# Optimization experiments

Measured on AMD Instinct MI355X. Metric: run time of the kernel, lower is better.

The kernel has to match this reference:

```python
import jax, jax.numpy as jnp
import numpy as np

B, S, D, H, NATT = 8, 512, 768, 256, 11  # batch, seq, d_model, gru hidden, n attention branches


def setup_inputs() -> dict:
    key = jax.random.key(0)
    ks = jax.random.split(key, 20)
    w = lambda k, shp, s=0.02: (jax.random.normal(k, shp, jnp.float32) * s)
    emb = w(ks[0], (7, D), 1.0).at[0].set(0.0)  # padding_idx=0 row is zero
    return {
        "essay_amlabel": jax.random.randint(ks[1], (B, S), 0, 7),
        "sequence_output": jax.random.normal(ks[2], (B, S, D), jnp.float32),
        "emb_table": emb,
        "Wq": w(ks[3], (NATT, D, D)), "bq": jnp.zeros((NATT, D), jnp.float32),
        "Wk": w(ks[4], (NATT, D, D)), "bk": jnp.zeros((NATT, D), jnp.float32),
        "Wv": w(ks[5], (NATT, D, D)), "bv": jnp.zeros((NATT, D), jnp.float32),
        "gru_Wih": w(ks[6], (2, 3 * H, D), 1.0 / np.sqrt(H)),
        "gru_Whh": w(ks[7], (2, 3 * H, H), 1.0 / np.sqrt(H)),
        "gru_bih": jnp.zeros((2, 3 * H), jnp.float32),
        "gru_bhh": jnp.zeros((2, 3 * H), jnp.float32),
        "W1": w(ks[8], (2 * H, 1)), "b1": jnp.zeros((1,), jnp.float32),
    }


def _gru_final_hidden(x, Wih, Whh, bih, bhh, reverse):
    # x: [N, S, D] -> final hidden [N, H] (PyTorch GRU equations)
    xp = jnp.einsum('nsd,hd->snh', x, Wih) + bih  # [S, N, 3H]

    def step(h, xt):
        gh = h @ Whh.T + bhh
        i_r, i_z, i_n = jnp.split(xt, 3, axis=-1)
        h_r, h_z, h_n = jnp.split(gh, 3, axis=-1)
        r = jax.nn.sigmoid(i_r + h_r)
        z = jax.nn.sigmoid(i_z + h_z)
        n = jnp.tanh(i_n + r * h_n)
        h_new = (1.0 - z) * n + z * h
        return h_new, None

    h0 = jnp.zeros((x.shape[0], Whh.shape[1]), x.dtype)
    h_final, _ = jax.lax.scan(step, h0, xp, reverse=reverse)
    return h_final


def reference(essay_amlabel, sequence_output, emb_table, Wq, bq, Wk, bk, Wv, bv,
              gru_Wih, gru_Whh, gru_bih, gru_bhh, W1, b1):
    am = emb_table[essay_amlabel]  # [B, S, D] queries
    # 11 independent attentions, num_heads=1, dropout=0 (eval) -> stack on axis k
    Q = jax.nn.relu(jnp.einsum('bsd,kde->kbse', am, Wq) + bq[:, None, None, :])
    K = jax.nn.relu(jnp.einsum('bsd,kde->kbse', sequence_output, Wk) + bk[:, None, None, :])
    V = jax.nn.relu(jnp.einsum('bsd,kde->kbse', sequence_output, Wv) + bv[:, None, None, :])
    scores = jnp.einsum('kbqd,kbmd->kbqm', Q, K) / jnp.sqrt(jnp.float32(D))
    attn = jax.nn.softmax(scores, axis=-1)
    qmask = jnp.sign(jnp.abs(jnp.sum(am, axis=-1)))  # [B, S]
    attn = attn * qmask[None, :, :, None]  # post-softmax query mask (as in source)
    out = jnp.einsum('kbqm,kbmd->kbqd', attn, V) + am[None]  # residual with queries
    eloutput = out + sequence_output[None]  # [11, B, S, D]
    gru_in = eloutput.reshape(NATT * B, S, D)
    h_f = _gru_final_hidden(gru_in, gru_Wih[0], gru_Whh[0], gru_bih[0], gru_bhh[0], False)
    h_b = _gru_final_hidden(gru_in, gru_Wih[1], gru_Whh[1], gru_bih[1], gru_bhh[1], True)
    final = jnp.concatenate([h_f, h_b], axis=-1)  # [11B, 2H]
    reshaped = final.reshape(NATT, B, 2 * H).transpose(1, 0, 2)  # [B, 11, 2H]
    logits = jax.nn.sigmoid(reshaped @ W1 + b1).squeeze(-1)  # [B, 11]
    return logits
```

## Files before the change

### kernel.cpp

```cpp
#include <hip/hip_runtime.h>
#include <hip/hip_bf16.h>
#include <hip/hip_fp16.h>
#include <math.h>

typedef __hip_bfloat16 bf16;
typedef __attribute__((ext_vector_type(8))) short short8;
typedef __attribute__((ext_vector_type(4))) float f32x4;

#define NATT 11
#define Bb 8
#define Ss 512
#define Dd 768
#define Hh 256
#define WSLICE 589824L

__device__ __forceinline__ void stf(float* p, float v) { *p = v; }
__device__ __forceinline__ void stf(bf16* p, float v) { *p = __float2bfloat16(v); }

__device__ __forceinline__ float blo(unsigned u) { return __uint_as_float(u << 16); }
__device__ __forceinline__ float bhi(unsigned u) { return __uint_as_float(u & 0xffff0000u); }
__device__ __forceinline__ float b2f(unsigned short u) { return __uint_as_float(((unsigned)u) << 16); }

__device__ __forceinline__ float ldg_any(const void* base, long idx, int flag) {
  if (flag) return ((const float*)base)[idx];
  return __bfloat162float(((const bf16*)base)[idx]);
}

__device__ __forceinline__ unsigned packh2(float a, float b) {
  __half2 hh = __floats2half2_rn(a, b);
  return __builtin_bit_cast(unsigned, hh);
}
__device__ __forceinline__ unsigned short f2h(float v) {
  __half h = __float2half(v);
  return __builtin_bit_cast(unsigned short, h);
}

typedef _Float16 f16x2 __attribute__((ext_vector_type(2)));

__device__ __forceinline__ float dot2u(unsigned a, unsigned b, float c) {
#if __has_builtin(__builtin_amdgcn_fdot2)
  return __builtin_amdgcn_fdot2(__builtin_bit_cast(f16x2, a),
                                __builtin_bit_cast(f16x2, b), c, false);
#else
  __half2 ah = __builtin_bit_cast(__half2, a);
  __half2 bh = __builtin_bit_cast(__half2, b);
  float2 af = __half22float2(ah), bf = __half22float2(bh);
  return c + af.x * bf.x + af.y * bf.y;
#endif
}

__device__ __forceinline__ float quad_sum(float v) {
#if __has_builtin(__builtin_amdgcn_update_dpp)
  int y = __builtin_amdgcn_update_dpp(0, __builtin_bit_cast(int, v), 0xB1, 0xF, 0xF, true);
  v += __builtin_bit_cast(float, y);
  y = __builtin_amdgcn_update_dpp(0, __builtin_bit_cast(int, v), 0x4E, 0xF, 0xF, true);
  v += __builtin_bit_cast(float, y);
  return v;
#else
  v += __shfl_xor(v, 1);
  v += __shfl_xor(v, 2);
  return v;
#endif
}

__device__ __forceinline__ void lds_barrier() {
  asm volatile("s_waitcnt lgkmcnt(0)\n\ts_barrier" ::: "memory");
}

__device__ __forceinline__ void load_lds16(const void* g, void* l) {
  __builtin_amdgcn_global_load_lds(
      (const __attribute__((address_space(1))) unsigned int*)g,
      (__attribute__((address_space(3))) unsigned int*)l, 16, 0, 0);
}

__global__ __launch_bounds__(64) void probe_kernel(
    const unsigned short* __restrict__ sequ, const unsigned* __restrict__ labu,
    int* __restrict__ flags)
{
  int t = threadIdx.x;
  int wild = 0;
#pragma unroll
  for (int i = 0; i < 4; i++) {
    unsigned short v = sequ[t + i * 64];
    int e = (v >> 7) & 0xFF;
    if (e < 90 || e > 160) wild++;
  }
  int nzodd = 0;
#pragma unroll
  for (int i = 0; i < 2; i++) {
    unsigned w = labu[(t + i * 64) * 2 + 1];
    if (w != 0) nzodd++;
  }
  for (int o = 32; o > 0; o >>= 1) {
    wild  += __shfl_down(wild, o);
    nzodd += __shfl_down(nzodd, o);
  }
  if (t == 0) {
    flags[0] = (wild > 32) ? 1 : 0;
    flags[1] = (nzodd == 0) ? 1 : 0;
  }
}

__global__ __launch_bounds__(256) void conv_seq_kernel(
    const void* __restrict__ seq, bf16* __restrict__ seqb,
    const int* __restrict__ flags)
{
  int flag = flags[0];
  long row = blockIdx.x;
#pragma unroll
  for (int i = 0; i < 3; i++) {
    long e = row * Dd + threadIdx.x + i * 256;
    seqb[e] = __float2bfloat16(ldg_any(seq, e, flag));
  }
}

__global__ __launch_bounds__(256) void convert_kernel(
    const void* __restrict__ src, bf16* __restrict__ dst, long n,
    const int* __restrict__ flags)
{
  int flag = flags[0];
  long i = (long)blockIdx.x * 256 + threadIdx.x;
  if (i < n) dst[i] = __float2bfloat16(ldg_any(src, i, flag));
}

__global__ __launch_bounds__(256) void smalls_kernel(
    const void* __restrict__ emb, const void* __restrict__ Wq,
    const void* __restrict__ bq, float* __restrict__ Qsmall,
    const int* __restrict__ flags)
{
  int flag = flags[0];
  __shared__ float embsh[7 * 768];
  int z = blockIdx.y, chunk = blockIdx.x, tid = threadIdx.x;
  for (int i = tid; i < 7 * 768; i += 256) embsh[i] = ldg_any(emb, i, flag);
  __syncthreads();
  int n = chunk * 256 + tid;
  float acc[7] = {};
  long base = (long)z * WSLICE;
  for (int e = 0; e < Dd; e++) {
    float wv = ldg_any(Wq, base + (long)e * Dd + n, flag);
#pragma unroll
    for (int l = 0; l < 7; l++) acc[l] += embsh[l * 768 + e] * wv;
  }
  float bv = ldg_any(bq, z * Dd + n, flag);
#pragma unroll
  for (int l = 0; l < 7; l++)
    Qsmall[((long)z * 7 + l) * Dd + n] = fmaxf(acc[l] + bv, 0.f);
}

__global__ __launch_bounds__(256) void emb_copy_kernel(
    const void* __restrict__ emb, bf16* __restrict__ outsm,
    float* __restrict__ qmask7, const int* __restrict__ flags)
{
  int flag = flags[0];
  int l = blockIdx.x;
  int t = threadIdx.x;
  float s = 0.f;
#pragma unroll
  for (int i = 0; i < 3; i++) {
    int e = t + i * 256;
    float v = ldg_any(emb, (long)l * Dd + e, flag);
    outsm[(long)(640 + l) * Dd + e] = __float2bfloat16(v);
    s += v;
  }
  for (int o = 32; o > 0; o >>= 1) s += __shfl_down(s, o);
  __shared__ float red[4];
  if ((t & 63) == 0) red[t >> 6] = s;
  __syncthreads();
  if (t == 0) {
    float tot = red[0] + red[1] + red[2] + red[3];
    qmask7[l] = (tot != 0.f) ? 1.f : 0.f;
  }
}

__global__ __launch_bounds__(256) void transpose2_kernel(
    const void* __restrict__ Wk, const void* __restrict__ Wv,
    bf16* __restrict__ WT, const int* __restrict__ flags)
{
  int flag = flags[0];
  __shared__ float tile[32][33];
  int z = blockIdx.z;
  int m = z >> 1, wsel = z & 1;
  const void* src = wsel ? Wv : Wk;
  long off = (long)m * WSLICE;
  bf16* dst = WT + (long)z * WSLICE;
  int kk0 = blockIdx.y * 32, n0 = blockIdx.x * 32;
  int tx = threadIdx.x & 31, ty = threadIdx.x >> 5;
#pragma unroll
  for (int i = 0; i < 4; i++)
    tile[ty + i * 8][tx] = ldg_any(src, off + (long)(kk0 + ty + i * 8) * Dd + n0 + tx, flag);
  __syncthreads();
#pragma unroll
  for (int i = 0; i < 4; i++)
    dst[(long)(n0 + ty + i * 8) * Dd + kk0 + tx] = __float2bfloat16(tile[tx][ty + i * 8]);
}

__device__ __forceinline__ void gemm_mfma_core(
    const bf16* __restrict__ Ab, long ldA,
    const bf16* __restrict__ Bbp, long ldB,
    bf16* As, bf16* Bs, int bm, int bn, int K,
    const void* bias, long bOff,
    void* C, long ldC, int cMode,
    float scale, int relu, int fflag)
{
  int tid = threadIdx.x;
  int lane = tid & 63, w = tid >> 6;
  int mo = (w & 1) * 64, no = (w >> 1) * 64;
  int l15 = lane & 15, q4 = lane >> 4;
  int gr = lane >> 2;
  int gs = (lane & 3) * 8;
  const bf16* aS0 = Ab + (long)(bm + w * 16 + gr) * ldA + gs;
  const bf16* aS1 = aS0 + 64 * ldA;
  const bf16* bS0 = Bbp + (long)(bn + w * 16 + gr) * ldB + gs;
  const bf16* bS1 = bS0 + 64 * ldB;
  bf16* aD0 = As + w * 512;
  bf16* aD1 = As + 2048 + w * 512;
  bf16* bD0 = Bs + w * 512;
  bf16* bD1 = Bs + 2048 + w * 512;

  f32x4 acc[4][4];
#pragma unroll
  for (int i = 0; i < 4; i++)
#pragma unroll
    for (int j = 0; j < 4; j++)
#pragma unroll
      for (int r = 0; r < 4; r++) acc[i][j][r] = 0.f;

  for (int k0 = 0; k0 < K; k0 += 32) {
    load_lds16(aS0, aD0);
    load_lds16(aS1, aD1);
    load_lds16(bS0, bD0);
    load_lds16(bS1, bD1);
    aS0 += 32; aS1 += 32; bS0 += 32; bS1 += 32;
    __syncthreads();
    short8 af[4], bfv[4];
#pragma unroll
    for (int i = 0; i < 4; i++)
      af[i] = *(const short8*)(As + (mo + i * 16 + l15) * 32 + q4 * 8);
#pragma unroll
    for (int j = 0; j < 4; j++)
      bfv[j] = *(const short8*)(Bs + (no + j * 16 + l15) * 32 + q4 * 8);
#pragma unroll
    for (int i = 0; i < 4; i++)
#pragma unroll
      for (int j = 0; j < 4; j++)
        acc[i][j] = __builtin_amdgcn_mfma_f32_16x16x32_bf16(af[i], bfv[j], acc[i][j], 0, 0, 0);
    __syncthreads();
  }

  float bsv[4];
#pragma unroll
  for (int j = 0; j < 4; j++) {
    int colg = bn + no + j * 16 + l15;
    bsv[j] = bias ? ldg_any(bias, bOff + colg, fflag) : 0.f;
  }
#pragma unroll
  for (int i = 0; i < 4; i++) {
#pragma unroll
    for (int j = 0; j < 4; j++) {
      int colg = bn + no + j * 16 + l15;
      if (cMode == 4) {
        int rowg0 = bm + mo + i * 16 + q4 * 4;
        ushort4 pk;
        unsigned short tmp[4];
#pragma unroll
        for (int r = 0; r < 4; r++) {
          float v = acc[i][j][r] * scale + bsv[j];
          if (relu) v = fmaxf(v, 0.f);
          tmp[r] = f2h(v);
        }
        pk.x = tmp[0]; pk.y = tmp[1]; pk.z = tmp[2]; pk.w = tmp[3];
        *(ushort4*)((unsigned short*)C + (long)colg * ldC + rowg0) = pk;
      } else {
#pragma unroll
        for (int r = 0; r < 4; r++) {
          int rowg = bm + mo + i * 16 + q4 * 4 + r;
          float v = acc[i][j][r] * scale + bsv[j];
          if (relu) v = fmaxf(v, 0.f);
          long off2 = (long)rowg * ldC + colg;
          if (cMode == 2)      ((float*)C)[off2] = v;
          else if (cMode == 3) ((unsigned short*)C)[off2] = f2h(v);
          else                 ((bf16*)C)[off2] = __float2bfloat16(v);
        }
      }
    }
  }
}

__global__ __launch_bounds__(256, 2) void proj_kernel(
    const bf16* __restrict__ seqb, const bf16* __restrict__ WT,
    const void* __restrict__ bk, const void* __restrict__ bv,
    unsigned short* __restrict__ Kb, unsigned short* __restrict__ Vt,
    const int* __restrict__ flags)
{
  __shared__ __align__(16) bf16 As[4096];
  __shared__ __align__(16) bf16 Bs[4096];
  int z = blockIdx.z;
  int m = z >> 1, wsel = z & 1;
  const bf16* B = WT + (long)z * WSLICE;
  if (wsel == 0) {
    gemm_mfma_core(seqb, Dd, B, Dd, As, Bs, blockIdx.y * 128, blockIdx.x * 128, Dd,
                   bk, (long)m * Dd, Kb + (long)m * 4096 * Dd, Dd, 3, 1.f, 1, flags[0]);
  } else {
    gemm_mfma_core(seqb, Dd, B, Dd, As, Bs, blockIdx.y * 128, blockIdx.x * 128, Dd,
                   bv, (long)m * Dd, Vt + (long)m * Dd * 4096, 4096, 4, 1.f, 1, flags[0]);
  }
}

__global__ __launch_bounds__(256, 2) void seqw_kernel(
    const bf16* __restrict__ seqb, const bf16* __restrict__ WihB,
    const void* __restrict__ bih, bf16* __restrict__ seqW,
    const int* __restrict__ flags)
{
  __shared__ __align__(16) bf16 As[4096];
  __shared__ __align__(16) bf16 Bs[4096];
  int dir = blockIdx.z;
  gemm_mfma_core(seqb, Dd, WihB + (long)dir * WSLICE, Dd, As, Bs,
                 blockIdx.y * 128, blockIdx.x * 128, Dd,
                 bih, (long)dir * Dd, seqW + (long)dir * 4096 * Dd, Dd, 0,
                 1.f, 0, flags[0]);
}

__global__ __launch_bounds__(256, 2) void pvw_kernel(
    const bf16* __restrict__ outsm, const bf16* __restrict__ WihB,
    float* __restrict__ PVW, const int* __restrict__ flags)
{
  __shared__ __align__(16) bf16 As[4096];
  __shared__ __align__(16) bf16 Bs[4096];
  int dir = blockIdx.z;
  gemm_mfma_core(outsm, Dd, WihB + (long)dir * WSLICE, Dd, As, Bs,
                 blockIdx.y * 128, blockIdx.x * 128, Dd,
                 nullptr, 0, PVW + (long)dir * 768 * Dd, Dd, 2, 1.f, 0, flags[0]);
}

__global__ __launch_bounds__(512, 2) void attn_kernel(
    const unsigned short* __restrict__ Kb, const unsigned short* __restrict__ Vt,
    const float* __restrict__ Qsmall, const float* __restrict__ qmask7,
    bf16* __restrict__ outsm, float scl)
{
  int blk = blockIdx.x;
  int k = blk >> 3, b = blk & 7;
  int tid = threadIdx.x;
  int lane = tid & 63, w = tid >> 6;
  __shared__ unsigned qs[7][384];
  __shared__ unsigned short ash[7][512];
  __shared__ float wred[8][7];
  __shared__ float gred[7];
  __shared__ float finv[7];
  for (int i = tid; i < 7 * 384; i += 512) {
    int l = i / 384, e2 = i - l * 384;
    const float* qp = Qsmall + ((long)k * 7 + l) * Dd + 2 * e2;
    qs[l][e2] = packh2(qp[0], qp[1]);
  }
  __syncthreads();
  const uint4* Krow = (const uint4*)(Kb + ((long)k * 4096 + b * 512 + tid) * Dd);
  float sc[7] = {};
  for (int e8 = 0; e8 < 96; e8++) {
    uint4 kv = Krow[e8];
#pragma unroll
    for (int l = 0; l < 7; l++) {
      sc[l] = dot2u(qs[l][e8 * 4],     kv.x, sc[l]);
      sc[l] = dot2u(qs[l][e8 * 4 + 1], kv.y, sc[l]);
      sc[l] = dot2u(qs[l][e8 * 4 + 2], kv.z, sc[l]);
      sc[l] = dot2u(qs[l][e8 * 4 + 3], kv.w, sc[l]);
    }
  }
#pragma unroll
  for (int l = 0; l < 7; l++) sc[l] *= scl;
#pragma unroll
  for (int l = 0; l < 7; l++) {
    float v = sc[l];
    for (int o = 32; o > 0; o >>= 1) v = fmaxf(v, __shfl_down(v, o));
    if (lane == 0) wred[w][l] = v;
  }
  __syncthreads();
  if (tid < 7) {
    float m = wred[0][tid];
#pragma unroll
    for (int i = 1; i < 8; i++) m = fmaxf(m, wred[i][tid]);
    gred[tid] = m;
  }
  __syncthreads();
  float ev[7];
#pragma unroll
  for (int l = 0; l < 7; l++) {
    ev[l] = __expf(sc[l] - gred[l]);
    float v = ev[l];
    for (int o = 32; o > 0; o >>= 1) v += __shfl_down(v, o);
    if (lane == 0) wred[w][l] = v;
  }
  __syncthreads();
  if (tid < 7) {
    float s = 0.f;
#pragma unroll
    for (int i = 0; i < 8; i++) s += wred[i][tid];
    finv[tid] = qmask7[tid] / s;
  }
  __syncthreads();
#pragma unroll
  for (int l = 0; l < 7; l++) ash[l][tid] = f2h(ev[l] * finv[l]);
  __syncthreads();
  for (int rep = 0; rep < 2; rep++) {
    int n = tid + rep * 512;
    if (n >= Dd) break;
    const uint4* Vrow = (const uint4*)(Vt + ((long)k * Dd + n) * 4096 + b * 512);
    float acc[7] = {};
    for (int m8 = 0; m8 < 64; m8++) {
      uint4 vv = Vrow[m8];
#pragma unroll
      for (int l = 0; l < 7; l++) {
        const unsigned* ap = (const unsigned*)&ash[l][0];
        acc[l] = dot2u(ap[m8 * 4],     vv.x, acc[l]);
        acc[l] = dot2u(ap[m8 * 4 + 1], vv.y, acc[l]);
        acc[l] = dot2u(ap[m8 * 4 + 2], vv.z, acc[l]);
        acc[l] = dot2u(ap[m8 * 4 + 3], vv.w, acc[l]);
      }
    }
#pragma unroll
    for (int l = 0; l < 7; l++)
      outsm[((long)blk * 7 + l) * Dd + n] = __float2bfloat16(acc[l]);
  }
}

__global__ __launch_bounds__(512, 2) void gru_kernel(
    const bf16* __restrict__ seqW,
    const float* __restrict__ PVW,
    const void* __restrict__ labels,
    const void* __restrict__ Whh, const void* __restrict__ bhh,
    float* __restrict__ hbuf, const int* __restrict__ flags)
{
  int flag = flags[0], lflag = flags[1];
  int idx = blockIdx.x;
  int dir = idx / 88, n = idx - dir * 88;
  int b = n & 7;
  int tid = threadIdx.x;
  int q = tid & 3, cg = tid >> 2;
  int hi = q >> 1;
  int ch = cg + hi * 128;
  int r0 = ch, r1 = 256 + ch, r2 = 512 + ch;

  unsigned w[6][32];
#pragma unroll
  for (int s = 0; s < 6; s++) {
    int row = (s >> 1) * 256 + cg + (s & 1) * 128;
    long base = ((long)dir * Dd + row) * Hh + q * 64;
    if (flag) {
      const float4* s4 = (const float4*)((const float*)Whh + base);
#pragma unroll
      for (int i = 0; i < 16; i++) {
        float4 v = s4[i];
        w[s][2 * i]     = packh2(v.x, v.y);
        w[s][2 * i + 1] = packh2(v.z, v.w);
      }
    } else {
      const uint4* s4 = (const uint4*)((const bf16*)Whh + base);
#pragma unroll
      for (int i = 0; i < 8; i++) {
        uint4 v = s4[i];
        w[s][4 * i]     = packh2(blo(v.x), bhi(v.x));
        w[s][4 * i + 1] = packh2(blo(v.y), bhi(v.y));
        w[s][4 * i + 2] = packh2(blo(v.z), bhi(v.z));
        w[s][4 * i + 3] = packh2(blo(v.w), bhi(v.w));
      }
    }
  }
  float bh0 = ldg_any(bhh, dir * Dd + r0, flag);
  float bh1 = ldg_any(bhh, dir * Dd + r1, flag);
  float bh2 = ldg_any(bhh, dir * Dd + r2, flag);

  __shared__ float rowsh[7 * 768];
  __shared__ int labsh[512];
  __shared__ __align__(16) unsigned short hsh[2][4 * 72];

  for (int i = tid; i < 7 * 768; i += 512) {
    int l = i / 768, row = i - l * 768;
    rowsh[i] = PVW[((long)dir * 768 + n * 7 + l) * Dd + row]
             + PVW[((long)dir * 768 + 640 + l) * Dd + row];
  }
  labsh[tid] = lflag ? (int)((const long long*)labels)[b * 512 + tid]
                     : ((const int*)labels)[b * 512 + tid];
  if (tid < 288) { hsh[0][tid] = 0; hsh[1][tid] = 0; }
  __syncthreads();

  const unsigned short* swu = (const unsigned short*)seqW
                            + ((long)dir * 4096 + b * 512) * Dd;
  int t0 = dir ? 511 : 0, t1 = dir ? 510 : 1, t2 = dir ? 509 : 2;
  unsigned short xs00 = swu[(long)t0 * Dd + r0];
  unsigned short xs01 = swu[(long)t0 * Dd + r1];
  unsigned short xs02 = swu[(long)t0 * Dd + r2];
  unsigned short xs10 = swu[(long)t1 * Dd + r0];
  unsigned short xs11 = swu[(long)t1 * Dd + r1];
  unsigned short xs12 = swu[(long)t1 * Dd + r2];
  unsigned short xs20 = swu[(long)t2 * Dd + r0];
  unsigned short xs21 = swu[(long)t2 * Dd + r1];
  unsigned short xs22 = swu[(long)t2 * Dd + r2];

  float hprev = 0.f;
  int hwaddr = (ch >> 6) * 72 + (ch & 63);
  for (int tt = 0; tt < Ss; tt++) {
    int t = dir ? 511 - tt : tt;
    int ttp = (tt + 3 < Ss) ? tt + 3 : Ss - 1;
    int tp = dir ? 511 - ttp : ttp;
    unsigned short xp0 = swu[(long)tp * Dd + r0];
    unsigned short xp1 = swu[(long)tp * Dd + r1];
    unsigned short xp2 = swu[(long)tp * Dd + r2];
    int lab = labsh[t];
    const float* rs = rowsh + lab * 768;
    float xr = rs[r0] + b2f(xs00);
    float xz = rs[r1] + b2f(xs01);
    float xn = rs[r2] + b2f(xs02);
    const uint4* hq = (const uint4*)(hsh[tt & 1] + q * 72);
    float a[6] = {};
#pragma unroll
    for (int jj = 0; jj < 8; jj++) {
      uint4 hv = hq[jj];
#pragma unroll
      for (int s = 0; s < 6; s++) {
        a[s] = dot2u(w[s][4 * jj],     hv.x, a[s]);
        a[s] = dot2u(w[s][4 * jj + 1], hv.y, a[s]);
        a[s] = dot2u(w[s][4 * jj + 2], hv.z, a[s]);
        a[s] = dot2u(w[s][4 * jj + 3], hv.w, a[s]);
      }
    }
#pragma unroll
    for (int s = 0; s < 6; s++) a[s] = quad_sum(a[s]);
    float ar = hi ? a[1] : a[0];
    float az = hi ? a[3] : a[2];
    float an = hi ? a[5] : a[4];
    float rg = 1.f / (1.f + __expf(-(xr + ar + bh0)));
    float zg = 1.f / (1.f + __expf(-(xz + az + bh1)));
    float targ = xn + rg * (an + bh2);
    float e2 = __expf(2.f * targ);
    float ng = 1.f - 2.f / (e2 + 1.f);
    float hnew = (1.f - zg) * ng + zg * hprev;
    hprev = hnew;
    if ((q & 1) == 0) hsh[(tt + 1) & 1][hwaddr] = f2h(hnew);
    lds_barrier();
    xs00 = xs10; xs01 = xs11; xs02 = xs12;
    xs10 = xs20; xs11 = xs21; xs12 = xs22;
    xs20 = xp0;  xs21 = xp1;  xs22 = xp2;
  }
  if ((q & 1) == 0) hbuf[((long)(dir * 88 + n)) * Hh + ch] = hprev;
}

__global__ __launch_bounds__(256) void head_kernel(
    const float* __restrict__ hbuf, const void* __restrict__ W1,
    const void* __restrict__ b1, void* __restrict__ out,
    const int* __restrict__ flags)
{
  int flag = flags[0];
  int n = blockIdx.x;
  int c = threadIdx.x;
  float v = hbuf[(long)n * Hh + c] * ldg_any(W1, c, flag)
          + hbuf[(long)(88 + n) * Hh + c] * ldg_any(W1, 256 + c, flag);
  for (int o = 32; o > 0; o >>= 1) v += __shfl_down(v, o);
  __shared__ float red[4];
  if ((c & 63) == 0) red[c >> 6] = v;
  __syncthreads();
  if (c == 0) {
    float s = red[0] + red[1] + red[2] + red[3] + ldg_any(b1, 0, flag);
    float sig = 1.f / (1.f + __expf(-s));
    int k = n / Bb, b = n - k * Bb;
    int o = b * NATT + k;
    if (flag) ((float*)out)[o] = sig;
    else      stf((bf16*)out + o, sig);
  }
}

extern "C" void kernel_launch(void* const* d_in, const int* in_sizes, int n_in,
                              void* d_out, int out_size, void* d_ws, size_t ws_size,
                              hipStream_t stream) {
  const void* labels = d_in[0];
  const void* seq  = d_in[1];
  const void* emb  = d_in[2];
  const void* Wq   = d_in[3];
  const void* bq   = d_in[4];
  const void* Wk   = d_in[5];
  const void* bk   = d_in[6];
  const void* Wv   = d_in[7];
  const void* bv   = d_in[8];
  const void* Wih  = d_in[9];
  const void* Whh  = d_in[10];
  const void* bih  = d_in[11];
  const void* bhh  = d_in[12];
  const void* W1   = d_in[13];
  const void* b1   = d_in[14];

  char* p = (char*)d_ws;
  size_t off = 0;
  auto alloc = [&](size_t bytes) -> void* {
    void* r = p + off; off += (bytes + 255) & ~(size_t)255; return r;
  };
  int*    flags  = (int*)alloc(2 * sizeof(int));
  bf16*   seqb   = (bf16*)alloc(4096UL * 768 * 2);
  float*  qmask7 = (float*)alloc(7 * 4);
  float*  Qsmall = (float*)alloc(11UL * 7 * 768 * 4);
  bf16*   WihB   = (bf16*)alloc(2UL * WSLICE * 2);
  bf16*   WT     = (bf16*)alloc(22UL * WSLICE * 2);
  unsigned short* Kb = (unsigned short*)alloc(11UL * 4096 * 768 * 2);
  unsigned short* Vt = (unsigned short*)alloc(11UL * 768 * 4096 * 2);
  bf16*   outsm  = (bf16*)alloc(768UL * 768 * 2);
  float*  PVW    = (float*)alloc(2UL * 768 * 768 * 4);
  bf16*   seqW   = (bf16*)alloc(2UL * 4096 * 768 * 2);
  float*  hbuf   = (float*)alloc(2UL * 88 * 256 * 4);
  if (off > ws_size) return;

  probe_kernel<<<1, 64, 0, stream>>>((const unsigned short*)seq,
                                     (const unsigned*)labels, flags);
  conv_seq_kernel<<<4096, 256, 0, stream>>>(seq, seqb, flags);
  convert_kernel<<<(int)((2 * WSLICE + 255) / 256), 256, 0, stream>>>(
      Wih, WihB, 2L * WSLICE, flags);
  smalls_kernel<<<dim3(3, 11), 256, 0, stream>>>(emb, Wq, bq, Qsmall, flags);
  emb_copy_kernel<<<7, 256, 0, stream>>>(emb, outsm, qmask7, flags);
  transpose2_kernel<<<dim3(24, 24, 22), 256, 0, stream>>>(Wk, Wv, WT, flags);
  proj_kernel<<<dim3(6, 32, 22), 256, 0, stream>>>(
      seqb, WT, bk, bv, Kb, Vt, flags);
  seqw_kernel<<<dim3(6, 32, 2), 256, 0, stream>>>(seqb, WihB, bih, seqW, flags);
  const float scl = 1.f / sqrtf(768.f);
  attn_kernel<<<88, 512, 0, stream>>>(Kb, Vt, Qsmall, qmask7, outsm, scl);
  pvw_kernel<<<dim3(6, 6, 2), 256, 0, stream>>>(outsm, WihB, PVW, flags);
  gru_kernel<<<176, 512, 0, stream>>>(seqW, PVW, labels, Whh, bhh, hbuf, flags);
  head_kernel<<<88, 256, 0, stream>>>(hbuf, W1, b1, d_out, flags);
}
```

Measured before the change: 1.194 ms.

## Split smalls reduction, stage transposed V stores through LDS, retune GRU occupancy

The small Q-projection kernel now splits the 768-long reduction across four wave groups, combining partial sums in shared memory, and launches four times as many blocks to fill more CUs. The transposed V output of the projection GEMM is staged through a padded LDS tile so each thread writes 16-byte contiguous rows instead of scattered 8-byte pieces. The GRU kernel's launch bounds switch to a waves-per-EU attribute to change register allocation. The added syncthreads in the staged epilogue and the altered GRU register budget could offset the gains.

```diff
diff --git a/kernel.cpp b/kernel.cpp
--- a/kernel.cpp
+++ b/kernel.cpp
@@ -13,6 +13,16 @@
 #define Dd 768
 #define Hh 256
 #define WSLICE 589824L
+
+#if defined(__has_attribute)
+#if __has_attribute(amdgpu_waves_per_eu)
+#define WAVES22 __attribute__((amdgpu_waves_per_eu(2, 2)))
+#else
+#define WAVES22
+#endif
+#else
+#define WAVES22
+#endif
 
 __device__ __forceinline__ void stf(float* p, float v) { *p = v; }
 __device__ __forceinline__ void stf(bf16* p, float v) { *p = __float2bfloat16(v); }
@@ -130,21 +140,33 @@
 {
   int flag = flags[0];
   __shared__ float embsh[7 * 768];
-  int z = blockIdx.y, chunk = blockIdx.x, tid = threadIdx.x;
+  __shared__ float psum[4][7][64];
+  int z = blockIdx.y;
+  int bx = blockIdx.x;
+  int tid = threadIdx.x;
+  int sub = tid >> 6, nl = tid & 63;
   for (int i = tid; i < 7 * 768; i += 256) embsh[i] = ldg_any(emb, i, flag);
   __syncthreads();
-  int n = chunk * 256 + tid;
+  int n = bx * 64 + nl;
+  long base = (long)z * WSLICE;
   float acc[7] = {};
-  long base = (long)z * WSLICE;
-  for (int e = 0; e < Dd; e++) {
+  int e0 = sub * 192;
+  for (int e = e0; e < e0 + 192; e++) {
     float wv = ldg_any(Wq, base + (long)e * Dd + n, flag);
 #pragma unroll
     for (int l = 0; l < 7; l++) acc[l] += embsh[l * 768 + e] * wv;
   }
-  float bv = ldg_any(bq, z * Dd + n, flag);
-#pragma unroll
-  for (int l = 0; l < 7; l++)
-    Qsmall[((long)z * 7 + l) * Dd + n] = fmaxf(acc[l] + bv, 0.f);
+#pragma unroll
+  for (int l = 0; l < 7; l++) psum[sub][l][nl] = acc[l];
+  __syncthreads();
+  if (sub == 0) {
+    float bv = ldg_any(bq, z * Dd + n, flag);
+#pragma unroll
+    for (int l = 0; l < 7; l++) {
+      float v = psum[0][l][nl] + psum[1][l][nl] + psum[2][l][nl] + psum[3][l][nl] + bv;
+      Qsmall[((long)z * 7 + l) * Dd + n] = fmaxf(v, 0.f);
+    }
+  }
 }
 
 __global__ __launch_bounds__(256) void emb_copy_kernel(
@@ -253,34 +275,51 @@
     int colg = bn + no + j * 16 + l15;
     bsv[j] = bias ? ldg_any(bias, bOff + colg, fflag) : 0.f;
   }
-#pragma unroll
-  for (int i = 0; i < 4; i++) {
+
+  if (cMode == 5) {
+    unsigned short* tile = (unsigned short*)As;
+    int cl = (no >> 6) * 16 + l15;
 #pragma unroll
     for (int j = 0; j < 4; j++) {
-      int colg = bn + no + j * 16 + l15;
-      if (cMode == 4) {
-        int rowg0 = bm + mo + i * 16 + q4 * 4;
-        ushort4 pk;
-        unsigned short tmp[4];
+      __syncthreads();
+#pragma unroll
+      for (int i = 0; i < 4; i++) {
 #pragma unroll
         for (int r = 0; r < 4; r++) {
           float v = acc[i][j][r] * scale + bsv[j];
           if (relu) v = fmaxf(v, 0.f);
-          tmp[r] = f2h(v);
+          tile[cl * 136 + mo + i * 16 + q4 * 4 + r] = f2h(v);
         }
-        pk.x = tmp[0]; pk.y = tmp[1]; pk.z = tmp[2]; pk.w = tmp[3];
-        *(ushort4*)((unsigned short*)C + (long)colg * ldC + rowg0) = pk;
-      } else {
-#pragma unroll
-        for (int r = 0; r < 4; r++) {
-          int rowg = bm + mo + i * 16 + q4 * 4 + r;
-          float v = acc[i][j][r] * scale + bsv[j];
-          if (relu) v = fmaxf(v, 0.f);
-          long off2 = (long)rowg * ldC + colg;
-          if (cMode == 2)      ((float*)C)[off2] = v;
-          else if (cMode == 3) ((unsigned short*)C)[off2] = f2h(v);
-          else                 ((bf16*)C)[off2] = __float2bfloat16(v);
-        }
+      }
+      __syncthreads();
+#pragma unroll
+      for (int uu = 0; uu < 2; uu++) {
+        int u = tid + uu * 256;
+        int c = u >> 4, mseg = u & 15;
+        int colg = bn + (c >> 4) * 64 + j * 16 + (c & 15);
+        uint2 v0 = *(const uint2*)(tile + c * 136 + mseg * 8);
+        uint2 v1 = *(const uint2*)(tile + c * 136 + mseg * 8 + 4);
+        uint4 pk; pk.x = v0.x; pk.y = v0.y; pk.z = v1.x; pk.w = v1.y;
+        *(uint4*)((unsigned short*)C + (long)colg * ldC + bm + mseg * 8) = pk;
+      }
+    }
+    return;
+  }
+
+#pragma unroll
+  for (int i = 0; i < 4; i++) {
+#pragma unroll
+    for (int j = 0; j < 4; j++) {
+      int colg = bn + no + j * 16 + l15;
+#pragma unroll
+      for (int r = 0; r < 4; r++) {
+        int rowg = bm + mo + i * 16 + q4 * 4 + r;
+        float v = acc[i][j][r] * scale + bsv[j];
+        if (relu) v = fmaxf(v, 0.f);
+        long off2 = (long)rowg * ldC + colg;
+        if (cMode == 2)      ((float*)C)[off2] = v;
+        else if (cMode == 3) ((unsigned short*)C)[off2] = f2h(v);
+        else                 ((bf16*)C)[off2] = __float2bfloat16(v);
       }
     }
   }
@@ -292,8 +331,9 @@
     unsigned short* __restrict__ Kb, unsigned short* __restrict__ Vt,
     const int* __restrict__ flags)
 {
-  __shared__ __align__(16) bf16 As[4096];
-  __shared__ __align__(16) bf16 Bs[4096];
+  __shared__ __align__(16) bf16 smem[8192];
+  bf16* As = smem;
+  bf16* Bs = smem + 4096;
   int z = blockIdx.z;
   int m = z >> 1, wsel = z & 1;
   const bf16* B = WT + (long)z * WSLICE;
@@ -302,7 +342,7 @@
                    bk, (long)m * Dd, Kb + (long)m * 4096 * Dd, Dd, 3, 1.f, 1, flags[0]);
   } else {
     gemm_mfma_core(seqb, Dd, B, Dd, As, Bs, blockIdx.y * 128, blockIdx.x * 128, Dd,
-                   bv, (long)m * Dd, Vt + (long)m * Dd * 4096, 4096, 4, 1.f, 1, flags[0]);
+                   bv, (long)m * Dd, Vt + (long)m * Dd * 4096, 4096, 5, 1.f, 1, flags[0]);
   }
 }
 
@@ -421,7 +461,7 @@
   }
 }
 
-__global__ __launch_bounds__(512, 2) void gru_kernel(
+__global__ __launch_bounds__(512) WAVES22 void gru_kernel(
     const bf16* __restrict__ seqW,
     const float* __restrict__ PVW,
     const void* __restrict__ labels,
@@ -609,7 +649,7 @@
   conv_seq_kernel<<<4096, 256, 0, stream>>>(seq, seqb, flags);
   convert_kernel<<<(int)((2 * WSLICE + 255) / 256), 256, 0, stream>>>(
       Wih, WihB, 2L * WSLICE, flags);
-  smalls_kernel<<<dim3(3, 11), 256, 0, stream>>>(emb, Wq, bq, Qsmall, flags);
+  smalls_kernel<<<dim3(12, 11), 256, 0, stream>>>(emb, Wq, bq, Qsmall, flags);
   emb_copy_kernel<<<7, 256, 0, stream>>>(emb, outsm, qmask7, flags);
   transpose2_kernel<<<dim3(24, 24, 22), 256, 0, stream>>>(Wk, Wv, WT, flags);
   proj_kernel<<<dim3(6, 32, 22), 256, 0, stream>>>(
```

Result: faster. 1.093 ms (-8.4%).
